# Kernel optimization log

Measured on AMD Instinct MI355X. Metric: run time of the kernel, lower is better.

## Reference

```python
import jax, jax.numpy as jnp
import numpy as np

N_NODE = 100_000
N_EDGE = 1_000_000
D = 64          # in_dim = out_dim
A = 64          # attn_dim
B = 8           # batchsize
N_REL = 200     # rel table size = 2*n_rel+1 = 401
N_ENT = 50_000
N_RELTAB = 2 * N_REL + 1


def setup_inputs() -> dict:
    key = jax.random.key(0)
    ks = jax.random.split(key, 16)
    # edges columns: [batch_query_idx, head_ent, rel, tail_ent, sub_local, obj_local]
    r_idx = jax.random.randint(ks[0], (N_EDGE,), 0, B)
    head = jax.random.randint(ks[1], (N_EDGE,), 0, N_ENT)
    rel = jax.random.randint(ks[2], (N_EDGE,), 0, N_RELTAB)
    tail = jax.random.randint(ks[3], (N_EDGE,), 0, N_ENT)
    sub = jax.random.randint(ks[4], (N_EDGE,), 0, N_NODE)
    obj = jax.random.randint(ks[5], (N_EDGE,), 0, N_NODE)
    edges = jnp.stack([r_idx, head, rel, tail, sub, obj], axis=1)
    nodes = jnp.stack([
        jax.random.randint(ks[6], (N_NODE,), 0, B),
        jax.random.randint(ks[7], (N_NODE,), 0, N_ENT)], axis=1)
    s = 1.0 / np.sqrt(D)
    return {
        "q_sub": jax.random.randint(ks[8], (B,), 0, N_ENT),
        "q_rel": jax.random.randint(ks[9], (B,), 0, N_RELTAB),
        "hidden": jax.random.normal(ks[10], (N_NODE, D), jnp.float32),
        "edges": edges,
        "nodes": nodes,
        "old_nodes_new_idx": jax.random.randint(ks[11], (50_000,), 0, N_NODE),
        "batchsize": B,
        "rel_emb": jax.random.normal(ks[12], (N_RELTAB, D), jnp.float32) * s,
        "Ws": jax.random.normal(ks[13], (A, D), jnp.float32) * s,
        "Wr": jax.random.normal(ks[14], (A, D), jnp.float32) * s,
        "Wqr_w": jax.random.normal(ks[15], (A, D), jnp.float32) * s,
        "Wqr_b": jnp.zeros((A,), jnp.float32),
        "walpha_w": jax.random.normal(jax.random.fold_in(key, 101), (1, A), jnp.float32) * (1.0 / np.sqrt(A)),
        "walpha_b": jnp.zeros((1,), jnp.float32),
        "Wh": jax.random.normal(jax.random.fold_in(key, 102), (D, D), jnp.float32) * s,
    }


def reference(q_sub, q_rel, hidden, edges, nodes, old_nodes_new_idx, batchsize,
              rel_emb, Ws, Wr, Wqr_w, Wqr_b, walpha_w, walpha_b, Wh):
    sub = edges[:, 4]   # local source node index [E]
    rel = edges[:, 2]   # relation index        [E]
    obj = edges[:, 5]   # local target node     [E]
    r_idx = edges[:, 0]  # which query each edge belongs to [E]

    hs = hidden[sub]                 # [E, D] gather of node hidden states
    hr = rel_emb[rel]                # [E, D] relation embedding (rela_embed(h, r) = rel_emb[r])
    h_qr = rel_emb[q_rel][r_idx]     # [E, D] query relation embedding per edge

    # attention MLP: sigmoid(w_alpha @ relu(Ws hs + Wr hr + Wqr h_qr + b))
    pre = (jnp.einsum('ed,ad->ea', hs, Ws)
           + jnp.einsum('ed,ad->ea', hr, Wr)
           + jnp.einsum('ed,ad->ea', h_qr, Wqr_w) + Wqr_b)        # [E, A]
    alpha = jax.nn.sigmoid(jnp.einsum('ea,oa->eo', jax.nn.relu(pre), walpha_w) + walpha_b)  # [E, 1]

    message = alpha * (hs + hr)      # [E, D]
    n_node = hidden.shape[0]
    message_agg = jax.ops.segment_sum(message, obj, num_segments=n_node)  # [N, D]
    hidden_new = jnp.einsum('nd,od->no', message_agg, Wh)  # act = identity
    return hidden_new
```

## Files before the change

### kernel.cpp

```cpp
#include <hip/hip_runtime.h>
#include <hip/hip_fp16.h>
#include <cstdint>
#include <cstddef>

#define DD 64
#define N_RELTAB 401
#define N_QR 8
#define T_ROWS (N_RELTAB + N_QR)
#define CHUNK 32
#define WPB 4

__device__ __forceinline__ uint16_t f2bf(float f) {
    uint32_t u = __float_as_uint(f);
    u += 0x7fffu + ((u >> 16) & 1u);
    return (uint16_t)(u >> 16);
}
__device__ __forceinline__ float bf2f(uint16_t u) {
    return __uint_as_float(((uint32_t)u) << 16);
}

__global__ __launch_bounds__(64) void build_C(
    const float* __restrict__ rel_emb, const float* __restrict__ Wr,
    const float* __restrict__ Wqr_w, const float* __restrict__ Wqr_b,
    const int* __restrict__ q_rel, float* __restrict__ Cf)
{
    int r = blockIdx.x, a = threadIdx.x;
    const float* w; const float* src; float acc;
    if (r < N_RELTAB) { w = Wr + a * DD; src = rel_emb + r * DD; acc = 0.f; }
    else {
        int k = r - N_RELTAB;
        w = Wqr_w + a * DD;
        src = rel_emb + q_rel[k] * DD;
        acc = Wqr_b[a];
    }
#pragma unroll
    for (int d = 0; d < DD; ++d) acc = fmaf(src[d], w[d], acc);
    Cf[r * DD + a] = acc;
}

template<bool BF16OUT>
__global__ __launch_bounds__(256) void rowmat_t(
    const float* __restrict__ in, const float* __restrict__ W,
    void* __restrict__ outv, int nrows)
{
    __shared__ float sIn[DD][DD + 1];
    int r0 = blockIdx.x * DD;
    int t = threadIdx.x;
    int vr = nrows - r0; if (vr > DD) vr = DD;

    const float4* gin = (const float4*)(in + (size_t)r0 * DD);
    int vf4 = vr * (DD / 4);
#pragma unroll
    for (int k = 0; k < 4; ++k) {
        int f = t + k * 256;
        float4 v = (f < vf4) ? gin[f] : make_float4(0.f, 0.f, 0.f, 0.f);
        int row = f >> 4, c4 = (f & 15) * 4;
        sIn[row][c4] = v.x; sIn[row][c4+1] = v.y; sIn[row][c4+2] = v.z; sIn[row][c4+3] = v.w;
    }
    __syncthreads();

    int row = t & 63, q = t >> 6;
    float acc[16];
#pragma unroll
    for (int c = 0; c < 16; ++c) acc[c] = 0.f;
    const float* wq = W + (q * 16) * DD;
    for (int d4 = 0; d4 < 16; ++d4) {
        float a0 = sIn[row][4*d4+0], a1 = sIn[row][4*d4+1];
        float a2 = sIn[row][4*d4+2], a3 = sIn[row][4*d4+3];
#pragma unroll
        for (int c = 0; c < 16; ++c) {
            const float* wr = wq + c * DD + d4 * 4;
            acc[c] = fmaf(a0, wr[0], acc[c]);
            acc[c] = fmaf(a1, wr[1], acc[c]);
            acc[c] = fmaf(a2, wr[2], acc[c]);
            acc[c] = fmaf(a3, wr[3], acc[c]);
        }
    }
    __syncthreads();

    if (BF16OUT) {
        uint32_t (*sOutU)[33] = (uint32_t (*)[33])&sIn[0][0];
#pragma unroll
        for (int c2 = 0; c2 < 8; ++c2)
            sOutU[row][q * 8 + c2] =
                (uint32_t)f2bf(acc[2*c2]) | ((uint32_t)f2bf(acc[2*c2+1]) << 16);
        __syncthreads();
        uint32_t* outU = (uint32_t*)outv;
        int vu = vr * (DD / 2);
#pragma unroll
        for (int k = 0; k < 8; ++k) {
            int u = t + k * 256;
            if (u < vu) outU[(size_t)r0 * (DD / 2) + u] = sOutU[u >> 5][u & 31];
        }
    } else {
#pragma unroll
        for (int c = 0; c < 16; ++c) sIn[row][q * 16 + c] = acc[c];
        __syncthreads();
        float4* out4 = (float4*)outv;
        int vf = vr * (DD / 4);
#pragma unroll
        for (int k = 0; k < 4; ++k) {
            int f = t + k * 256;
            if (f < vf) {
                int rr = f >> 4, c4 = (f & 15) * 4;
                float4 v;
                v.x = sIn[rr][c4]; v.y = sIn[rr][c4+1];
                v.z = sIn[rr][c4+2]; v.w = sIn[rr][c4+3];
                out4[(size_t)r0 * (DD / 4) + f] = v;
            }
        }
    }
}

__global__ __launch_bounds__(256) void hist_emit(
    const int* __restrict__ edges, int* __restrict__ counts,
    uint64_t* __restrict__ keys, int n_edge)
{
    int e = blockIdx.x * 256 + threadIdx.x;
    if (e >= n_edge) return;
    const int2* ep = (const int2*)(edges + 6 * e);
    int ridx = ep[0].x;
    int rel  = ep[1].x;
    int2 so  = ep[2];
    atomicAdd(&counts[so.y], 1);
    uint32_t pay = (uint32_t)so.x | ((uint32_t)rel << 17) | ((uint32_t)ridx << 26);
    keys[e] = (uint64_t)pay | ((uint64_t)(uint32_t)so.y << 32);
}

__global__ __launch_bounds__(1024) void scan1(
    const int* __restrict__ counts, int* __restrict__ offsets,
    int* __restrict__ bsums, int n)
{
    __shared__ int wsum[16];
    int t = threadIdx.x, i = blockIdx.x * 1024 + t;
    int lane = t & 63, wid = t >> 6;
    int c = (i < n) ? counts[i] : 0;
    int v = c;
#pragma unroll
    for (int d = 1; d < 64; d <<= 1) { int u = __shfl_up(v, d); if (lane >= d) v += u; }
    if (lane == 63) wsum[wid] = v;
    __syncthreads();
    if (wid == 0) {
        int s = (lane < 16) ? wsum[lane] : 0;
#pragma unroll
        for (int d = 1; d < 16; d <<= 1) { int u = __shfl_up(s, d); if (lane >= d) s += u; }
        if (lane < 16) wsum[lane] = s;
    }
    __syncthreads();
    int woff = (wid == 0) ? 0 : wsum[wid - 1];
    if (i < n) offsets[i] = woff + v - c;
    if (t == 1023) bsums[blockIdx.x] = wsum[15];
}

__global__ __launch_bounds__(1024) void scan_small(
    const int* __restrict__ bsums, int* __restrict__ boffs, int nb)
{
    __shared__ int wsum[16];
    int t = threadIdx.x, lane = t & 63, wid = t >> 6;
    int c = (t < nb) ? bsums[t] : 0;
    int v = c;
#pragma unroll
    for (int d = 1; d < 64; d <<= 1) { int u = __shfl_up(v, d); if (lane >= d) v += u; }
    if (lane == 63) wsum[wid] = v;
    __syncthreads();
    if (wid == 0) {
        int s = (lane < 16) ? wsum[lane] : 0;
#pragma unroll
        for (int d = 1; d < 16; d <<= 1) { int u = __shfl_up(s, d); if (lane >= d) s += u; }
        if (lane < 16) wsum[lane] = s;
    }
    __syncthreads();
    int woff = (wid == 0) ? 0 : wsum[wid - 1];
    if (t < nb) boffs[t] = woff + v - c;
}

__global__ __launch_bounds__(1024) void scan3(
    int* __restrict__ offsets, int* __restrict__ cursor,
    const int* __restrict__ boffs, int n)
{
    int i = blockIdx.x * 1024 + threadIdx.x;
    if (i < n) {
        int v = offsets[i] + boffs[blockIdx.x];
        offsets[i] = v;
        cursor[i] = v;
    }
}

__global__ __launch_bounds__(256) void build_sorted(
    const uint64_t* __restrict__ keys, int* __restrict__ cursor,
    uint64_t* __restrict__ sorted, int n_edge)
{
    int e = blockIdx.x * 256 + threadIdx.x;
    if (e >= n_edge) return;
    uint64_t k = keys[e];
    int obj = (int)(k >> 32);
    int pos = atomicAdd(&cursor[obj], 1);
    sorted[pos] = k;
}

__global__ __launch_bounds__(256, 4) void fused_aggregate(
    const uint64_t* __restrict__ sorted, const uint16_t* __restrict__ Xb,
    const float* __restrict__ hidden, const float* __restrict__ Cf,
    const float* __restrict__ rel_emb, const float* __restrict__ walpha_w,
    const float* __restrict__ walpha_b, float* __restrict__ agg,
    int n_edge, int n_node)
{
    __shared__ float sQ[N_QR * DD];
    __shared__ __half sS[WPB][CHUNK][DD + 2];
    int tid = threadIdx.x, lane = tid & 63, wid = tid >> 6;
    for (int i = tid; i < N_QR * DD; i += 64 * WPB) sQ[i] = Cf[N_RELTAB * DD + i];
    __syncthreads();

    long chunk = (long)blockIdx.x * WPB + wid;
    long base = chunk * CHUNK;
    if (base >= n_edge) return;

    int e_l = (int)base + (lane & 31);
    uint64_t k = (lane < 32 && e_l < n_edge)
                     ? sorted[e_l]
                     : ((uint64_t)(uint32_t)n_node << 32);
    uint32_t pay = (uint32_t)k;
    int obj      = (int)(k >> 32);

    float wa = walpha_w[lane];
    float wb = walpha_b[0];

#pragma unroll 8
    for (int j = 0; j < CHUNK; ++j) {
        uint32_t pj = (uint32_t)__builtin_amdgcn_readlane((int)pay, j);
        int sub  = (int)(pj & 0x1FFFFu);
        int rel  = (int)((pj >> 17) & 0x1FFu);
        int ridx = (int)((pj >> 26) & 7u);
        float x = bf2f(Xb[((size_t)sub << 6) + lane]);
        float c = Cf[(rel << 6) + lane];
        float q = sQ[(ridx << 6) + lane];
        sS[wid][j][lane] = __float2half(fmaxf(x + c + q, 0.f) * wa);
    }

    int eb = lane & 31, hb = lane >> 5;
    const __half2* row2 = (const __half2*)&sS[wid][eb][hb * 32];
    float tsum = 0.f;
#pragma unroll
    for (int a2 = 0; a2 < 16; ++a2) {
        float2 f = __half22float2(row2[a2]);
        tsum += f.x + f.y;
    }
    tsum += __shfl_xor(tsum, 32);
    float alpha = 1.f / (1.f + __expf(-(tsum + wb)));

    float acc = 0.f;
    int prev = __builtin_amdgcn_readlane(obj, 0);
    bool first = true;
#pragma unroll 4
    for (int j = 0; j < CHUNK; ++j) {
        int oj = __builtin_amdgcn_readlane(obj, j);
        if (oj != prev) {
            if (prev < n_node) {
                float* dst = &agg[((size_t)prev << 6) + lane];
                if (first) atomicAdd(dst, acc); else *dst = acc;
            }
            first = false; acc = 0.f; prev = oj;
        }
        if (oj < n_node) {
            uint32_t pj = (uint32_t)__builtin_amdgcn_readlane((int)pay, j);
            int sub = (int)(pj & 0x1FFFFu);
            int rel = (int)((pj >> 17) & 0x1FFu);
            float h = hidden[((size_t)sub << 6) + lane];
            float r = rel_emb[(rel << 6) + lane];
            float aj = __uint_as_float(
                (uint32_t)__builtin_amdgcn_readlane((int)__float_as_uint(alpha), j));
            acc = fmaf(aj, h + r, acc);
        }
    }
    if (prev < n_node) atomicAdd(&agg[((size_t)prev << 6) + lane], acc);
}

extern "C" void kernel_launch(void* const* d_in, const int* in_sizes, int n_in,
                              void* d_out, int out_size, void* d_ws, size_t ws_size,
                              hipStream_t stream)
{
    const int*   q_rel    = (const int*)d_in[1];
    const float* hidden   = (const float*)d_in[2];
    const int*   edges    = (const int*)d_in[3];
    const float* rel_emb  = (const float*)d_in[7];
    const float* Ws       = (const float*)d_in[8];
    const float* Wr       = (const float*)d_in[9];
    const float* Wqr_w    = (const float*)d_in[10];
    const float* Wqr_b    = (const float*)d_in[11];
    const float* walpha_w = (const float*)d_in[12];
    const float* walpha_b = (const float*)d_in[13];
    const float* Wh       = (const float*)d_in[14];
    float* out = (float*)d_out;

    const int n_node = in_sizes[2] / DD;
    const int n_edge = in_sizes[3] / 6;
    const int NB = (n_node + 1023) / 1024;

    char* w = (char*)d_ws;
    uint16_t* Xb      = (uint16_t*)w;  w += (size_t)n_node * DD * 2;
    float*    agg     = (float*)w;     w += (size_t)n_node * DD * 4;
    uint64_t* sorted  = (uint64_t*)w;  w += (size_t)n_edge * 8;
    uint64_t* keys    = (uint64_t*)w;  w += (size_t)n_edge * 8;
    int*      counts  = (int*)w;       w += (size_t)n_node * 4;
    int*      offsets = (int*)w;       w += (size_t)n_node * 4;
    int*      cursor  = (int*)w;       w += (size_t)n_node * 4;
    int*      bsums   = (int*)w;       w += 4096;
    int*      boffs   = (int*)w;       w += 4096;
    float*    Cf      = (float*)w;     w += (size_t)T_ROWS * DD * 4;

    build_C<<<T_ROWS, 64, 0, stream>>>(rel_emb, Wr, Wqr_w, Wqr_b, q_rel, Cf);
    rowmat_t<true><<<(n_node + DD - 1) / DD, 256, 0, stream>>>(hidden, Ws, Xb, n_node);
    hipMemsetAsync(counts, 0, (size_t)n_node * 4, stream);
    hipMemsetAsync(agg, 0, (size_t)n_node * DD * 4, stream);
    hist_emit<<<(n_edge + 255) / 256, 256, 0, stream>>>(edges, counts, keys, n_edge);
    scan1<<<NB, 1024, 0, stream>>>(counts, offsets, bsums, n_node);
    scan_small<<<1, 1024, 0, stream>>>(bsums, boffs, NB);
    scan3<<<NB, 1024, 0, stream>>>(offsets, cursor, boffs, n_node);
    build_sorted<<<(n_edge + 255) / 256, 256, 0, stream>>>(keys, cursor, sorted, n_edge);
    const int nchunks = (n_edge + CHUNK - 1) / CHUNK;
    fused_aggregate<<<(nchunks + WPB - 1) / WPB, 64 * WPB, 0, stream>>>(
        sorted, Xb, hidden, Cf, rel_emb, walpha_w, walpha_b, agg, n_edge, n_node);
    rowmat_t<false><<<(n_node + DD - 1) / DD, 256, 0, stream>>>(agg, Wh, out, n_node);
}
```

Measured before the change: 428.3 us.

## Apply Wh before aggregation and scatter directly into output

Uses linearity to move the final Wh projection ahead of the segment sum: hidden·Wh and rel_emb·Wh are precomputed, so the aggregation writes straight into the output buffer. This removes the separate agg buffer and the final node-level matmul pass. The sort now stores 4-byte payloads plus a node-of-position array filled by a new per-node kernel, and hist_emit reads edges as int4 pairs. The cost is a second matmul in the prep kernel, an extra fp32 HWh table write, and summation order changes from reassociation.

```diff
diff --git a/kernel.cpp b/kernel.cpp
--- a/kernel.cpp
+++ b/kernel.cpp
@@ -19,29 +19,41 @@
     return __uint_as_float(((uint32_t)u) << 16);
 }
 
-__global__ __launch_bounds__(64) void build_C(
+__global__ __launch_bounds__(64) void build_tables(
     const float* __restrict__ rel_emb, const float* __restrict__ Wr,
     const float* __restrict__ Wqr_w, const float* __restrict__ Wqr_b,
-    const int* __restrict__ q_rel, float* __restrict__ Cf)
+    const int* __restrict__ q_rel, const float* __restrict__ Wh,
+    float* __restrict__ Cf, float* __restrict__ RWh)
 {
     int r = blockIdx.x, a = threadIdx.x;
-    const float* w; const float* src; float acc;
-    if (r < N_RELTAB) { w = Wr + a * DD; src = rel_emb + r * DD; acc = 0.f; }
-    else {
+    if (r < N_RELTAB) {
+        const float* src = rel_emb + r * DD;
+        const float* w1 = Wr + a * DD;
+        const float* w2 = Wh + a * DD;
+        float a1 = 0.f, a2 = 0.f;
+#pragma unroll
+        for (int d = 0; d < DD; ++d) {
+            float s = src[d];
+            a1 = fmaf(s, w1[d], a1);
+            a2 = fmaf(s, w2[d], a2);
+        }
+        Cf[r * DD + a] = a1;
+        RWh[r * DD + a] = a2;
+    } else {
         int k = r - N_RELTAB;
-        w = Wqr_w + a * DD;
-        src = rel_emb + q_rel[k] * DD;
-        acc = Wqr_b[a];
-    }
-#pragma unroll
-    for (int d = 0; d < DD; ++d) acc = fmaf(src[d], w[d], acc);
-    Cf[r * DD + a] = acc;
-}
-
-template<bool BF16OUT>
-__global__ __launch_bounds__(256) void rowmat_t(
-    const float* __restrict__ in, const float* __restrict__ W,
-    void* __restrict__ outv, int nrows)
+        const float* src = rel_emb + q_rel[k] * DD;
+        const float* w = Wqr_w + a * DD;
+        float acc = Wqr_b[a];
+#pragma unroll
+        for (int d = 0; d < DD; ++d) acc = fmaf(src[d], w[d], acc);
+        Cf[r * DD + a] = acc;
+    }
+}
+
+__global__ __launch_bounds__(256) void prep(
+    const float* __restrict__ in, const float* __restrict__ Ws,
+    const float* __restrict__ Wh, uint16_t* __restrict__ Xb,
+    float* __restrict__ HWh, int nrows)
 {
     __shared__ float sIn[DD][DD + 1];
     int r0 = blockIdx.x * DD;
@@ -60,43 +72,52 @@
     __syncthreads();
 
     int row = t & 63, q = t >> 6;
-    float acc[16];
-#pragma unroll
-    for (int c = 0; c < 16; ++c) acc[c] = 0.f;
-    const float* wq = W + (q * 16) * DD;
+    float accX[16], accH[16];
+#pragma unroll
+    for (int c = 0; c < 16; ++c) { accX[c] = 0.f; accH[c] = 0.f; }
+    const float* wqX = Ws + (q * 16) * DD;
+    const float* wqH = Wh + (q * 16) * DD;
     for (int d4 = 0; d4 < 16; ++d4) {
         float a0 = sIn[row][4*d4+0], a1 = sIn[row][4*d4+1];
         float a2 = sIn[row][4*d4+2], a3 = sIn[row][4*d4+3];
 #pragma unroll
         for (int c = 0; c < 16; ++c) {
-            const float* wr = wq + c * DD + d4 * 4;
-            acc[c] = fmaf(a0, wr[0], acc[c]);
-            acc[c] = fmaf(a1, wr[1], acc[c]);
-            acc[c] = fmaf(a2, wr[2], acc[c]);
-            acc[c] = fmaf(a3, wr[3], acc[c]);
-        }
-    }
-    __syncthreads();
-
-    if (BF16OUT) {
+            const float* wx = wqX + c * DD + d4 * 4;
+            const float* wh = wqH + c * DD + d4 * 4;
+            accX[c] = fmaf(a0, wx[0], accX[c]);
+            accX[c] = fmaf(a1, wx[1], accX[c]);
+            accX[c] = fmaf(a2, wx[2], accX[c]);
+            accX[c] = fmaf(a3, wx[3], accX[c]);
+            accH[c] = fmaf(a0, wh[0], accH[c]);
+            accH[c] = fmaf(a1, wh[1], accH[c]);
+            accH[c] = fmaf(a2, wh[2], accH[c]);
+            accH[c] = fmaf(a3, wh[3], accH[c]);
+        }
+    }
+    __syncthreads();
+
+    {
         uint32_t (*sOutU)[33] = (uint32_t (*)[33])&sIn[0][0];
 #pragma unroll
         for (int c2 = 0; c2 < 8; ++c2)
             sOutU[row][q * 8 + c2] =
-                (uint32_t)f2bf(acc[2*c2]) | ((uint32_t)f2bf(acc[2*c2+1]) << 16);
+                (uint32_t)f2bf(accX[2*c2]) | ((uint32_t)f2bf(accX[2*c2+1]) << 16);
         __syncthreads();
-        uint32_t* outU = (uint32_t*)outv;
+        uint32_t* outU = (uint32_t*)Xb;
         int vu = vr * (DD / 2);
 #pragma unroll
         for (int k = 0; k < 8; ++k) {
             int u = t + k * 256;
             if (u < vu) outU[(size_t)r0 * (DD / 2) + u] = sOutU[u >> 5][u & 31];
         }
-    } else {
-#pragma unroll
-        for (int c = 0; c < 16; ++c) sIn[row][q * 16 + c] = acc[c];
+    }
+    __syncthreads();
+
+    {
+#pragma unroll
+        for (int c = 0; c < 16; ++c) sIn[row][q * 16 + c] = accH[c];
         __syncthreads();
-        float4* out4 = (float4*)outv;
+        float4* out4 = (float4*)HWh;
         int vf = vr * (DD / 4);
 #pragma unroll
         for (int k = 0; k < 4; ++k) {
@@ -113,18 +134,25 @@
 }
 
 __global__ __launch_bounds__(256) void hist_emit(
-    const int* __restrict__ edges, int* __restrict__ counts,
+    const int4* __restrict__ edges4, int* __restrict__ counts,
     uint64_t* __restrict__ keys, int n_edge)
 {
-    int e = blockIdx.x * 256 + threadIdx.x;
-    if (e >= n_edge) return;
-    const int2* ep = (const int2*)(edges + 6 * e);
-    int ridx = ep[0].x;
-    int rel  = ep[1].x;
-    int2 so  = ep[2];
-    atomicAdd(&counts[so.y], 1);
-    uint32_t pay = (uint32_t)so.x | ((uint32_t)rel << 17) | ((uint32_t)ridx << 26);
-    keys[e] = (uint64_t)pay | ((uint64_t)(uint32_t)so.y << 32);
+    int t = blockIdx.x * 256 + threadIdx.x;
+    int e0 = 2 * t;
+    if (e0 >= n_edge) return;
+    int4 a = edges4[3 * t];
+    int4 b = edges4[3 * t + 1];
+    {
+        uint32_t pay = (uint32_t)b.x | ((uint32_t)a.z << 17) | ((uint32_t)a.x << 26);
+        atomicAdd(&counts[b.y], 1);
+        keys[e0] = (uint64_t)pay | ((uint64_t)(uint32_t)b.y << 32);
+    }
+    if (e0 + 1 < n_edge) {
+        int4 c = edges4[3 * t + 2];
+        uint32_t pay = (uint32_t)c.z | ((uint32_t)c.x << 17) | ((uint32_t)b.z << 26);
+        atomicAdd(&counts[c.w], 1);
+        keys[e0 + 1] = (uint64_t)pay | ((uint64_t)(uint32_t)c.w << 32);
+    }
 }
 
 __global__ __launch_bounds__(1024) void scan1(
@@ -186,24 +214,34 @@
     }
 }
 
+__global__ __launch_bounds__(256) void fill_runs(
+    const int* __restrict__ offsets, const int* __restrict__ counts,
+    uint32_t* __restrict__ node_of_pos, int n_node)
+{
+    int n = blockIdx.x * 256 + threadIdx.x;
+    if (n >= n_node) return;
+    int s = offsets[n], c = counts[n];
+    for (int i = 0; i < c; ++i) node_of_pos[s + i] = (uint32_t)n;
+}
+
 __global__ __launch_bounds__(256) void build_sorted(
     const uint64_t* __restrict__ keys, int* __restrict__ cursor,
-    uint64_t* __restrict__ sorted, int n_edge)
+    uint32_t* __restrict__ sorted_pay, int n_edge)
 {
     int e = blockIdx.x * 256 + threadIdx.x;
     if (e >= n_edge) return;
     uint64_t k = keys[e];
     int obj = (int)(k >> 32);
     int pos = atomicAdd(&cursor[obj], 1);
-    sorted[pos] = k;
+    sorted_pay[pos] = (uint32_t)k;
 }
 
 __global__ __launch_bounds__(256, 4) void fused_aggregate(
-    const uint64_t* __restrict__ sorted, const uint16_t* __restrict__ Xb,
-    const float* __restrict__ hidden, const float* __restrict__ Cf,
-    const float* __restrict__ rel_emb, const float* __restrict__ walpha_w,
-    const float* __restrict__ walpha_b, float* __restrict__ agg,
-    int n_edge, int n_node)
+    const uint32_t* __restrict__ sorted_pay, const uint32_t* __restrict__ node_of_pos,
+    const uint16_t* __restrict__ Xb, const float* __restrict__ HWh,
+    const float* __restrict__ Cf, const float* __restrict__ RWh,
+    const float* __restrict__ walpha_w, const float* __restrict__ walpha_b,
+    float* __restrict__ out, int n_edge, int n_node)
 {
     __shared__ float sQ[N_QR * DD];
     __shared__ __half sS[WPB][CHUNK][DD + 2];
@@ -216,11 +254,12 @@
     if (base >= n_edge) return;
 
     int e_l = (int)base + (lane & 31);
-    uint64_t k = (lane < 32 && e_l < n_edge)
-                     ? sorted[e_l]
-                     : ((uint64_t)(uint32_t)n_node << 32);
-    uint32_t pay = (uint32_t)k;
-    int obj      = (int)(k >> 32);
+    uint32_t pay = 0;
+    int obj = n_node;
+    if (lane < 32 && e_l < n_edge) {
+        pay = sorted_pay[e_l];
+        obj = (int)node_of_pos[e_l];
+    }
 
     float wa = walpha_w[lane];
     float wb = walpha_b[0];
@@ -251,12 +290,12 @@
     float acc = 0.f;
     int prev = __builtin_amdgcn_readlane(obj, 0);
     bool first = true;
-#pragma unroll 4
+#pragma unroll 8
     for (int j = 0; j < CHUNK; ++j) {
         int oj = __builtin_amdgcn_readlane(obj, j);
         if (oj != prev) {
             if (prev < n_node) {
-                float* dst = &agg[((size_t)prev << 6) + lane];
+                float* dst = &out[((size_t)prev << 6) + lane];
                 if (first) atomicAdd(dst, acc); else *dst = acc;
             }
             first = false; acc = 0.f; prev = oj;
@@ -265,14 +304,14 @@
             uint32_t pj = (uint32_t)__builtin_amdgcn_readlane((int)pay, j);
             int sub = (int)(pj & 0x1FFFFu);
             int rel = (int)((pj >> 17) & 0x1FFu);
-            float h = hidden[((size_t)sub << 6) + lane];
-            float r = rel_emb[(rel << 6) + lane];
+            float h = HWh[((size_t)sub << 6) + lane];
+            float r = RWh[(rel << 6) + lane];
             float aj = __uint_as_float(
                 (uint32_t)__builtin_amdgcn_readlane((int)__float_as_uint(alpha), j));
             acc = fmaf(aj, h + r, acc);
         }
     }
-    if (prev < n_node) atomicAdd(&agg[((size_t)prev << 6) + lane], acc);
+    if (prev < n_node) atomicAdd(&out[((size_t)prev << 6) + lane], acc);
 }
 
 extern "C" void kernel_launch(void* const* d_in, const int* in_sizes, int n_in,
@@ -298,27 +337,32 @@
 
     char* w = (char*)d_ws;
     uint16_t* Xb      = (uint16_t*)w;  w += (size_t)n_node * DD * 2;
-    float*    agg     = (float*)w;     w += (size_t)n_node * DD * 4;
-    uint64_t* sorted  = (uint64_t*)w;  w += (size_t)n_edge * 8;
+    float*    HWh     = (float*)w;     w += (size_t)n_node * DD * 4;
     uint64_t* keys    = (uint64_t*)w;  w += (size_t)n_edge * 8;
+    uint32_t* spay    = (uint32_t*)w;  w += (size_t)n_edge * 4;
+    uint32_t* npos    = (uint32_t*)w;  w += (size_t)n_edge * 4;
     int*      counts  = (int*)w;       w += (size_t)n_node * 4;
     int*      offsets = (int*)w;       w += (size_t)n_node * 4;
     int*      cursor  = (int*)w;       w += (size_t)n_node * 4;
     int*      bsums   = (int*)w;       w += 4096;
     int*      boffs   = (int*)w;       w += 4096;
     float*    Cf      = (float*)w;     w += (size_t)T_ROWS * DD * 4;
-
-    build_C<<<T_ROWS, 64, 0, stream>>>(rel_emb, Wr, Wqr_w, Wqr_b, q_rel, Cf);
-    rowmat_t<true><<<(n_node + DD - 1) / DD, 256, 0, stream>>>(hidden, Ws, Xb, n_node);
+    float*    RWh     = (float*)w;     w += (size_t)N_RELTAB * DD * 4;
+
+    build_tables<<<T_ROWS, 64, 0, stream>>>(rel_emb, Wr, Wqr_w, Wqr_b, q_rel, Wh,
+                                            Cf, RWh);
+    prep<<<(n_node + DD - 1) / DD, 256, 0, stream>>>(hidden, Ws, Wh, Xb, HWh, n_node);
     hipMemsetAsync(counts, 0, (size_t)n_node * 4, stream);
-    hipMemsetAsync(agg, 0, (size_t)n_node * DD * 4, stream);
-    hist_emit<<<(n_edge + 255) / 256, 256, 0, stream>>>(edges, counts, keys, n_edge);
+    hipMemsetAsync(out, 0, (size_t)out_size * 4, stream);
+    const int npair = (n_edge + 1) / 2;
+    hist_emit<<<(npair + 255) / 256, 256, 0, stream>>>(
+        (const int4*)edges, counts, keys, n_edge);
     scan1<<<NB, 1024, 0, stream>>>(counts, offsets, bsums, n_node);
     scan_small<<<1, 1024, 0, stream>>>(bsums, boffs, NB);
     scan3<<<NB, 1024, 0, stream>>>(offsets, cursor, boffs, n_node);
-    build_sorted<<<(n_edge + 255) / 256, 256, 0, stream>>>(keys, cursor, sorted, n_edge);
+    fill_runs<<<(n_node + 255) / 256, 256, 0, stream>>>(offsets, counts, npos, n_node);
+    build_sorted<<<(n_edge + 255) / 256, 256, 0, stream>>>(keys, cursor, spay, n_edge);
     const int nchunks = (n_edge + CHUNK - 1) / CHUNK;
     fused_aggregate<<<(nchunks + WPB - 1) / WPB, 64 * WPB, 0, stream>>>(
-        sorted, Xb, hidden, Cf, rel_emb, walpha_w, walpha_b, agg, n_edge, n_node);
-    rowmat_t<false><<<(n_node + DD - 1) / DD, 256, 0, stream>>>(agg, Wh, out, n_node);
-}
+        spay, npos, Xb, HWh, Cf, RWh, walpha_w, walpha_b, out, n_edge, n_node);
+}
```

New measurement: 421.6 us. About the same (-1.6%).
